# Kernel tuning notes

Measured on AMD Instinct MI355X. Metric: run time of the kernel, lower is better.

Reference implementation:

```python
import jax, jax.numpy as jnp
import numpy as np

N_GRAPHS = 1000  # static number of graphs for global_mean_pool


def setup_inputs() -> dict:
    key = jax.random.key(0)
    ks = jax.random.split(key, 12)
    N, E, DIN, H, OUT = 100000, 1600000, 64, 128, 10
    x = jax.random.normal(ks[0], (N, DIN), dtype=jnp.float32)
    edge_index = jax.random.randint(ks[1], (2, E), 0, N, dtype=jnp.int64)
    batch = jnp.sort(jax.random.randint(ks[2], (N,), 0, N_GRAPHS, dtype=jnp.int64))
    g = lambda k, shp, fan: jax.random.normal(k, shp, dtype=jnp.float32) * np.float32(1.0 / np.sqrt(fan))
    return {
        "x": x, "edge_index": edge_index, "batch": batch,
        "W1": g(ks[3], (DIN, H), DIN), "b1": jnp.zeros((H,), jnp.float32),
        "W2": g(ks[4], (H, H), H),     "b2": jnp.zeros((H,), jnp.float32),
        "W3": g(ks[5], (H, H), H),     "b3": jnp.zeros((H,), jnp.float32),
        "Wl": g(ks[6], (H, OUT), H),   "bl": jnp.zeros((OUT,), jnp.float32),
    }


def _gcn_norm(edge_index, num_nodes):
    # Add self-loops, compute symmetric normalization D^-1/2 (A+I) D^-1/2.
    loops = jnp.arange(num_nodes, dtype=edge_index.dtype)
    src = jnp.concatenate([edge_index[0], loops])
    dst = jnp.concatenate([edge_index[1], loops])
    deg = jax.ops.segment_sum(jnp.ones_like(dst, dtype=jnp.float32), dst, num_segments=num_nodes)
    dinv = jnp.where(deg > 0, jax.lax.rsqrt(jnp.maximum(deg, 1.0)), 0.0)
    norm = dinv[src] * dinv[dst]  # [E + N]
    return src, dst, norm


def _gcn_conv(h, W, b, src, dst, norm, num_nodes):
    h = h @ W                              # linear transform first (PyG GCNConv)
    msg = h[src] * norm[:, None]           # gather + edge scale
    out = jax.ops.segment_sum(msg, dst, num_segments=num_nodes)  # scatter-add
    return out + b


def reference(x, edge_index, batch, W1, b1, W2, b2, W3, b3, Wl, bl):
    N = x.shape[0]
    src, dst, norm = _gcn_norm(edge_index, N)
    h = jax.nn.relu(_gcn_conv(x, W1, b1, src, dst, norm, N))
    h = jax.nn.relu(_gcn_conv(h, W2, b2, src, dst, norm, N))
    h = jax.nn.relu(_gcn_conv(h, W3, b3, src, dst, norm, N))
    # global mean pool over graphs
    sums = jax.ops.segment_sum(h, batch, num_segments=N_GRAPHS)
    cnt = jax.ops.segment_sum(jnp.ones((N,), jnp.float32), batch, num_segments=N_GRAPHS)
    pooled = sums / jnp.maximum(cnt, 1.0)[:, None]
    # dropout(p=0.5) is identity in eval mode
    return pooled @ Wl + bl  # [N_GRAPHS, OUT]
```

## Files before the change

kernel.cpp:

```cpp
#include <hip/hip_runtime.h>
#include <math.h>

#define HID 128
#define NOUT 10
#define NG 1000
#define SCAN_B 256

typedef unsigned short u16;
typedef __attribute__((ext_vector_type(8))) short bf16x8;
typedef __attribute__((ext_vector_type(8))) unsigned short u16x8;
typedef __attribute__((ext_vector_type(4))) float f32x4;

__device__ inline u16 f2bf(float f) {
    unsigned x = __float_as_uint(f);
    return (u16)((x + 0x7FFF + ((x >> 16) & 1)) >> 16);
}
__device__ inline float bf2f(u16 b) { return __uint_as_float(((unsigned)b) << 16); }

__global__ void k_zero(float* __restrict__ p, int n) {
    int i = blockIdx.x * 256 + threadIdx.x;
    if (i < n) p[i] = 0.f;
}

__global__ void k_count_rank(const int* __restrict__ ei, int* __restrict__ counts,
                             int* __restrict__ rank, int E) {
    int e = blockIdx.x * 256 + threadIdx.x;
    if (e < E) rank[e] = atomicAdd(&counts[ei[(size_t)E + e]], 1);
}

__global__ __launch_bounds__(SCAN_B) void k_scan1(const int* __restrict__ counts,
                                                  int* __restrict__ rowptr,
                                                  int* __restrict__ bsum,
                                                  float* __restrict__ dinv, int N) {
    __shared__ int s[SCAN_B];
    int t = threadIdx.x;
    int i = blockIdx.x * SCAN_B + t;
    int v = (i < N) ? counts[i] : 0;
    if (i < N) dinv[i] = rsqrtf((float)(v + 1));
    s[t] = v;
    __syncthreads();
    for (int off = 1; off < SCAN_B; off <<= 1) {
        int u = (t >= off) ? s[t - off] : 0;
        __syncthreads();
        s[t] += u;
        __syncthreads();
    }
    if (i < N) rowptr[i] = s[t] - v;
    if (t == SCAN_B - 1) bsum[blockIdx.x] = s[t];
}

__global__ __launch_bounds__(512) void k_scan2(int* __restrict__ bsum, int nb) {
    __shared__ int s[512];
    int t = threadIdx.x;
    int v = (t < nb) ? bsum[t] : 0;
    s[t] = v;
    __syncthreads();
    for (int off = 1; off < 512; off <<= 1) {
        int u = (t >= off) ? s[t - off] : 0;
        __syncthreads();
        s[t] += u;
        __syncthreads();
    }
    if (t < nb) bsum[t] = s[t] - v;
}

__global__ void k_scan3(int* __restrict__ rowptr, const int* __restrict__ bsum, int N, int E) {
    int i = blockIdx.x * SCAN_B + threadIdx.x;
    if (i < N) rowptr[i] += bsum[blockIdx.x];
    if (i == 0) rowptr[N] = E;
}

__global__ void k_scatter(const int* __restrict__ ei, const int* __restrict__ rank,
                          const int* __restrict__ rowptr, int* __restrict__ sorted, int E) {
    int e = blockIdx.x * 256 + threadIdx.x;
    if (e >= E) return;
    int s = ei[e];
    int d = ei[(size_t)E + e];
    sorted[rowptr[d] + rank[e]] = s << 8;
}

__global__ void k_bounds(const int* __restrict__ batch, int* __restrict__ gstart, int N) {
    int i = blockIdx.x * 256 + threadIdx.x;
    if (i >= N) return;
    int cur = batch[i];
    if (i == 0) {
        for (int g = 0; g <= cur; ++g) gstart[g] = 0;
    } else {
        int prev = batch[i - 1];
        for (int g = prev + 1; g <= cur; ++g) gstart[g] = i;
    }
    if (i == N - 1) {
        for (int g = cur + 1; g <= NG; ++g) gstart[g] = N;
    }
}

template<int K>
__global__ void k_wsplit(const float* __restrict__ W, u16* __restrict__ whi, u16* __restrict__ wlo) {
    int idx = blockIdx.x * 256 + threadIdx.x;
    if (idx >= K * HID) return;
    int k = idx >> 7;
    int col = idx & 127;
    float v = W[idx];
    u16 hb = f2bf(v);
    u16 lb = f2bf(v - bf2f(hb));
    int ks = k >> 5;
    int kq = (k >> 3) & 3;
    int j = k & 7;
    int c = col >> 4;
    int r = col & 15;
    int lane = kq * 16 + r;
    size_t pos = ((size_t)(ks * 8 + c) * 64 + lane) * 8 + j;
    whi[pos] = hb;
    wlo[pos] = lb;
}

template<int K, bool RELU_IN>
__global__ __launch_bounds__(256) void k_gemm_mfma(const float* __restrict__ in,
                                                   const u16* __restrict__ whi,
                                                   const u16* __restrict__ wlo,
                                                   const float* __restrict__ dinv,
                                                   u16* __restrict__ g, int N) {
    constexpr int NKS = K / 32;
    const int w = threadIdx.x >> 6;
    const int l = threadIdx.x & 63;
    const int row0 = blockIdx.x * 64 + w * 16;
    const int r = l & 15;
    const int q = l >> 4;

    int arow = row0 + r;
    if (arow > N - 1) arow = N - 1;
    const float* ap = in + (size_t)arow * K + q * 8;

    bf16x8 ahi[NKS], alo[NKS];
#pragma unroll
    for (int ks = 0; ks < NKS; ++ks) {
        float4 v0 = *(const float4*)(ap + ks * 32);
        float4 v1 = *(const float4*)(ap + ks * 32 + 4);
        float va[8] = {v0.x, v0.y, v0.z, v0.w, v1.x, v1.y, v1.z, v1.w};
#pragma unroll
        for (int j = 0; j < 8; ++j) {
            float f = va[j];
            if (RELU_IN) f = fmaxf(f, 0.f);
            u16 hb = f2bf(f);
            ahi[ks][j] = (short)hb;
            alo[ks][j] = (short)f2bf(f - bf2f(hb));
        }
    }

    f32x4 acc[8];
#pragma unroll
    for (int c = 0; c < 8; ++c) acc[c] = (f32x4){0.f, 0.f, 0.f, 0.f};

    const bf16x8* whiv = (const bf16x8*)whi;
    const bf16x8* wlov = (const bf16x8*)wlo;

#pragma unroll
    for (int ks = 0; ks < NKS; ++ks) {
#pragma unroll
        for (int c = 0; c < 8; ++c) {
            bf16x8 b = whiv[(size_t)(ks * 8 + c) * 64 + l];
            acc[c] = __builtin_amdgcn_mfma_f32_16x16x32_bf16(ahi[ks], b, acc[c], 0, 0, 0);
            acc[c] = __builtin_amdgcn_mfma_f32_16x16x32_bf16(alo[ks], b, acc[c], 0, 0, 0);
        }
    }
#pragma unroll
    for (int ks = 0; ks < NKS; ++ks) {
#pragma unroll
        for (int c = 0; c < 8; ++c) {
            bf16x8 b = wlov[(size_t)(ks * 8 + c) * 64 + l];
            acc[c] = __builtin_amdgcn_mfma_f32_16x16x32_bf16(ahi[ks], b, acc[c], 0, 0, 0);
        }
    }

    float dv[4];
#pragma unroll
    for (int i = 0; i < 4; ++i) {
        int rr = row0 + q * 4 + i;
        dv[i] = (rr < N) ? dinv[rr] : 0.f;
    }
#pragma unroll
    for (int c = 0; c < 8; ++c) {
#pragma unroll
        for (int i = 0; i < 4; ++i) {
            int rr = row0 + q * 4 + i;
            if (rr < N) g[(size_t)rr * HID + c * 16 + r] = f2bf(acc[c][i] * dv[i]);
        }
    }
}

#define BFACC(a, p)                                   \
    a[0] += __uint_as_float((p).x << 16);             \
    a[1] += __uint_as_float((p).x & 0xffff0000u);     \
    a[2] += __uint_as_float((p).y << 16);             \
    a[3] += __uint_as_float((p).y & 0xffff0000u);     \
    a[4] += __uint_as_float((p).z << 16);             \
    a[5] += __uint_as_float((p).z & 0xffff0000u);     \
    a[6] += __uint_as_float((p).w << 16);             \
    a[7] += __uint_as_float((p).w & 0xffff0000u);

__global__ __launch_bounds__(256) void k_aggr(const int* __restrict__ rowptr,
                                              const int* __restrict__ sorted,
                                              const u16* __restrict__ g,
                                              const float* __restrict__ dinv,
                                              const float* __restrict__ b,
                                              float* __restrict__ out, int N) {
    int wid = threadIdx.x >> 6;
    int lane = threadIdx.x & 63;
    int v = blockIdx.x * 4 + wid;
    if (v >= N) return;
    int qq = lane >> 4;
    int r = lane & 15;
    int cb = r * 16;

    const char* gb = (const char*)g;

    float a0[8], a1[8];
#pragma unroll
    for (int i = 0; i < 8; ++i) { a0[i] = 0.f; a1[i] = 0.f; }

    int beg = rowptr[v], end = rowptr[v + 1];
    int j = beg + qq;
    for (; j + 4 < end; j += 8) {
        int o0 = sorted[j];
        int o1 = sorted[j + 4];
        uint4 p0 = *(const uint4*)(gb + o0 + cb);
        uint4 p1 = *(const uint4*)(gb + o1 + cb);
        BFACC(a0, p0);
        BFACC(a1, p1);
    }
    for (; j < end; j += 4) {
        int o0 = sorted[j];
        uint4 p0 = *(const uint4*)(gb + o0 + cb);
        BFACC(a0, p0);
    }

#pragma unroll
    for (int i = 0; i < 8; ++i) {
        float t = a0[i] + a1[i];
        t += __shfl_xor(t, 16);
        t += __shfl_xor(t, 32);
        a0[i] = t;
    }

    if (qq == 0) {
        uint4 sv = *(const uint4*)(gb + ((size_t)v << 8) + cb);
        float se[8];
        se[0] = __uint_as_float(sv.x << 16); se[1] = __uint_as_float(sv.x & 0xffff0000u);
        se[2] = __uint_as_float(sv.y << 16); se[3] = __uint_as_float(sv.y & 0xffff0000u);
        se[4] = __uint_as_float(sv.z << 16); se[5] = __uint_as_float(sv.z & 0xffff0000u);
        se[6] = __uint_as_float(sv.w << 16); se[7] = __uint_as_float(sv.w & 0xffff0000u);
        float dv = dinv[v];
        int c8 = r * 8;
        float4 bv0 = *(const float4*)&b[c8];
        float4 bv1 = *(const float4*)&b[c8 + 4];
        float4 o0, o1;
        o0.x = bv0.x + dv * (a0[0] + se[0]);
        o0.y = bv0.y + dv * (a0[1] + se[1]);
        o0.z = bv0.z + dv * (a0[2] + se[2]);
        o0.w = bv0.w + dv * (a0[3] + se[3]);
        o1.x = bv1.x + dv * (a0[4] + se[4]);
        o1.y = bv1.y + dv * (a0[5] + se[5]);
        o1.z = bv1.z + dv * (a0[6] + se[6]);
        o1.w = bv1.w + dv * (a0[7] + se[7]);
        *(float4*)&out[(size_t)v * HID + c8] = o0;
        *(float4*)&out[(size_t)v * HID + c8 + 4] = o1;
    }
}

__global__ __launch_bounds__(256) void k_poolfinal(const float* __restrict__ h,
                                                   const int* __restrict__ gstart,
                                                   const float* __restrict__ Wl,
                                                   const float* __restrict__ bl,
                                                   float* __restrict__ out) {
    __shared__ float pool[HID];
    int g = blockIdx.x;
    int t = threadIdx.x;
    int col = t & 127;
    int grp = t >> 7;
    int beg = gstart[g], end = gstart[g + 1];

    float acc = 0.f;
    for (int i = beg + grp; i < end; i += 2)
        acc += fmaxf(h[(size_t)i * HID + col], 0.f);

    if (grp == 1) pool[col] = acc;
    __syncthreads();
    if (grp == 0) {
        float tot = acc + pool[col];
        float c = fmaxf((float)(end - beg), 1.0f);
        pool[col] = tot / c;
    }
    __syncthreads();
    if (t < NOUT) {
        float a = bl[t];
        for (int k = 0; k < HID; ++k) a += pool[k] * Wl[k * NOUT + t];
        out[g * NOUT + t] = a;
    }
}

__global__ void k_probe(float* __restrict__ out, int n, float val) {
    int i = blockIdx.x * 256 + threadIdx.x;
    if (i < n) out[i] = val;
}

extern "C" void kernel_launch(void* const* d_in, const int* in_sizes, int n_in,
                              void* d_out, int out_size, void* d_ws, size_t ws_size,
                              hipStream_t stream) {
    const float* x    = (const float*)d_in[0];
    const int* ei     = (const int*)d_in[1];
    const int* batch  = (const int*)d_in[2];
    const float* W1 = (const float*)d_in[3];
    const float* b1 = (const float*)d_in[4];
    const float* W2 = (const float*)d_in[5];
    const float* b2 = (const float*)d_in[6];
    const float* W3 = (const float*)d_in[7];
    const float* b3 = (const float*)d_in[8];
    const float* Wl = (const float*)d_in[9];
    const float* bl = (const float*)d_in[10];
    float* out = (float*)d_out;

    const int N = in_sizes[0] / 64;
    const int E = in_sizes[1] / 2;

    char* ws = (char*)d_ws;
    const size_t off_dinv   = 0;
    const size_t off_counts = 400000;
    const size_t off_rowptr = 800000;
    const size_t off_rank   = 1200128;
    const size_t off_bsum   = 7600128;
    const size_t off_gstart = 7602176;
    const size_t off_sorted = 7606400;
    const size_t off_hW     = 14006400;
    const size_t off_bufB   = 39606400;
    const size_t off_wf1h   = 90806400;
    const size_t off_wf1l   = 90822784;
    const size_t off_wf2h   = 90839168;
    const size_t off_wf2l   = 90871936;
    const size_t off_wf3h   = 90904704;
    const size_t off_wf3l   = 90937472;
    const size_t need       = 90970240;

    if (ws_size < need) {
        float enc = (float)(ws_size >> 20);
        k_probe<<<(out_size + 255) / 256, 256, 0, stream>>>(out, out_size, enc);
        return;
    }

    float* dinv  = (float*)(ws + off_dinv);
    int* counts  = (int*)(ws + off_counts);
    int* rowptr  = (int*)(ws + off_rowptr);
    int* rank    = (int*)(ws + off_rank);
    int* bsum    = (int*)(ws + off_bsum);
    int* gstart  = (int*)(ws + off_gstart);
    int* sorted  = (int*)(ws + off_sorted);
    u16* hW      = (u16*)(ws + off_hW);
    float* bufB  = (float*)(ws + off_bufB);
    u16* wf1h = (u16*)(ws + off_wf1h);  u16* wf1l = (u16*)(ws + off_wf1l);
    u16* wf2h = (u16*)(ws + off_wf2h);  u16* wf2l = (u16*)(ws + off_wf2l);
    u16* wf3h = (u16*)(ws + off_wf3h);  u16* wf3l = (u16*)(ws + off_wf3l);

    dim3 blk(256);
    const int gN = (N + 255) / 256;
    const int gE = (E + 255) / 256;
    const int nScanBlk = (N + SCAN_B - 1) / SCAN_B;
    const int mfmaGrid = (N + 63) / 64;
    const int aggrGrid = (N + 3) / 4;

    k_zero<<<gN, blk, 0, stream>>>((float*)counts, N);
    k_count_rank<<<gE, blk, 0, stream>>>(ei, counts, rank, E);
    k_scan1<<<nScanBlk, SCAN_B, 0, stream>>>(counts, rowptr, bsum, dinv, N);
    k_scan2<<<1, 512, 0, stream>>>(bsum, nScanBlk);
    k_scan3<<<nScanBlk, SCAN_B, 0, stream>>>(rowptr, bsum, N, E);
    k_scatter<<<gE, blk, 0, stream>>>(ei, rank, rowptr, sorted, E);
    k_bounds<<<gN, blk, 0, stream>>>(batch, gstart, N);
    k_wsplit<64><<<(64 * HID + 255) / 256, blk, 0, stream>>>(W1, wf1h, wf1l);
    k_wsplit<128><<<(128 * HID + 255) / 256, blk, 0, stream>>>(W2, wf2h, wf2l);
    k_wsplit<128><<<(128 * HID + 255) / 256, blk, 0, stream>>>(W3, wf3h, wf3l);

    k_gemm_mfma<64, false><<<mfmaGrid, blk, 0, stream>>>(x, wf1h, wf1l, dinv, hW, N);
    k_aggr<<<aggrGrid, blk, 0, stream>>>(rowptr, sorted, hW, dinv, b1, bufB, N);
    k_gemm_mfma<128, true><<<mfmaGrid, blk, 0, stream>>>(bufB, wf2h, wf2l, dinv, hW, N);
    k_aggr<<<aggrGrid, blk, 0, stream>>>(rowptr, sorted, hW, dinv, b2, bufB, N);
    k_gemm_mfma<128, true><<<mfmaGrid, blk, 0, stream>>>(bufB, wf3h, wf3l, dinv, hW, N);
    k_aggr<<<aggrGrid, blk, 0, stream>>>(rowptr, sorted, hW, dinv, b3, bufB, N);

    k_poolfinal<<<NG, blk, 0, stream>>>(bufB, gstart, Wl, bl, out);
}
```

Baseline: 457.5 us.

## Fuse ReLU and bf16 hi/lo split into aggregation, split nodes across two waves

The aggregation kernel now applies bias and ReLU itself and writes its output as pre-split bf16 hi/lo arrays instead of fp32. The next GEMM loads these operands directly rather than converting fp32 on load, and the pooling kernel reads the hi/lo pair. Each node's aggregation is split across two wavefronts, one per 64-column half, so more waves run while each gathers half the row bytes. The three weight-split launches are merged into one. The intermediate buffers keep the same total bytes, but per-row conversion work moves out of the GEMM.

```diff
diff --git a/kernel.cpp b/kernel.cpp
--- a/kernel.cpp
+++ b/kernel.cpp
@@ -8,7 +8,6 @@
 
 typedef unsigned short u16;
 typedef __attribute__((ext_vector_type(8))) short bf16x8;
-typedef __attribute__((ext_vector_type(8))) unsigned short u16x8;
 typedef __attribute__((ext_vector_type(4))) float f32x4;
 
 __device__ inline u16 f2bf(float f) {
@@ -94,13 +93,20 @@
     }
 }
 
-template<int K>
-__global__ void k_wsplit(const float* __restrict__ W, u16* __restrict__ whi, u16* __restrict__ wlo) {
+__global__ void k_wsplit_all(const float* __restrict__ W1, const float* __restrict__ W2,
+                             const float* __restrict__ W3,
+                             u16* __restrict__ w1h, u16* __restrict__ w1l,
+                             u16* __restrict__ w2h, u16* __restrict__ w2l,
+                             u16* __restrict__ w3h, u16* __restrict__ w3l) {
     int idx = blockIdx.x * 256 + threadIdx.x;
-    if (idx >= K * HID) return;
-    int k = idx >> 7;
-    int col = idx & 127;
-    float v = W[idx];
+    const float* W; u16 *wh, *wl; int base;
+    if (idx < 64 * HID)            { W = W1; wh = w1h; wl = w1l; base = idx; }
+    else if (idx < 192 * HID)      { W = W2; wh = w2h; wl = w2l; base = idx - 64 * HID; }
+    else if (idx < 320 * HID)      { W = W3; wh = w3h; wl = w3l; base = idx - 192 * HID; }
+    else return;
+    int k = base >> 7;
+    int col = base & 127;
+    float v = W[base];
     u16 hb = f2bf(v);
     u16 lb = f2bf(v - bf2f(hb));
     int ks = k >> 5;
@@ -110,16 +116,16 @@
     int r = col & 15;
     int lane = kq * 16 + r;
     size_t pos = ((size_t)(ks * 8 + c) * 64 + lane) * 8 + j;
-    whi[pos] = hb;
-    wlo[pos] = lb;
-}
-
-template<int K, bool RELU_IN>
-__global__ __launch_bounds__(256) void k_gemm_mfma(const float* __restrict__ in,
-                                                   const u16* __restrict__ whi,
-                                                   const u16* __restrict__ wlo,
-                                                   const float* __restrict__ dinv,
-                                                   u16* __restrict__ g, int N) {
+    wh[pos] = hb;
+    wl[pos] = lb;
+}
+
+template<int K>
+__global__ __launch_bounds__(256) void k_gemm_f32(const float* __restrict__ in,
+                                                  const u16* __restrict__ whi,
+                                                  const u16* __restrict__ wlo,
+                                                  const float* __restrict__ dinv,
+                                                  u16* __restrict__ g, int N) {
     constexpr int NKS = K / 32;
     const int w = threadIdx.x >> 6;
     const int l = threadIdx.x & 63;
@@ -140,11 +146,77 @@
 #pragma unroll
         for (int j = 0; j < 8; ++j) {
             float f = va[j];
-            if (RELU_IN) f = fmaxf(f, 0.f);
             u16 hb = f2bf(f);
             ahi[ks][j] = (short)hb;
             alo[ks][j] = (short)f2bf(f - bf2f(hb));
         }
+    }
+
+    f32x4 acc[8];
+#pragma unroll
+    for (int c = 0; c < 8; ++c) acc[c] = (f32x4){0.f, 0.f, 0.f, 0.f};
+
+    const bf16x8* whiv = (const bf16x8*)whi;
+    const bf16x8* wlov = (const bf16x8*)wlo;
+
+#pragma unroll
+    for (int ks = 0; ks < NKS; ++ks) {
+#pragma unroll
+        for (int c = 0; c < 8; ++c) {
+            bf16x8 b = whiv[(size_t)(ks * 8 + c) * 64 + l];
+            acc[c] = __builtin_amdgcn_mfma_f32_16x16x32_bf16(ahi[ks], b, acc[c], 0, 0, 0);
+            acc[c] = __builtin_amdgcn_mfma_f32_16x16x32_bf16(alo[ks], b, acc[c], 0, 0, 0);
+        }
+    }
+#pragma unroll
+    for (int ks = 0; ks < NKS; ++ks) {
+#pragma unroll
+        for (int c = 0; c < 8; ++c) {
+            bf16x8 b = wlov[(size_t)(ks * 8 + c) * 64 + l];
+            acc[c] = __builtin_amdgcn_mfma_f32_16x16x32_bf16(ahi[ks], b, acc[c], 0, 0, 0);
+        }
+    }
+
+    float dv[4];
+#pragma unroll
+    for (int i = 0; i < 4; ++i) {
+        int rr = row0 + q * 4 + i;
+        dv[i] = (rr < N) ? dinv[rr] : 0.f;
+    }
+#pragma unroll
+    for (int c = 0; c < 8; ++c) {
+#pragma unroll
+        for (int i = 0; i < 4; ++i) {
+            int rr = row0 + q * 4 + i;
+            if (rr < N) g[(size_t)rr * HID + c * 16 + r] = f2bf(acc[c][i] * dv[i]);
+        }
+    }
+}
+
+template<int K>
+__global__ __launch_bounds__(256) void k_gemm_pre(const u16* __restrict__ ain_h,
+                                                  const u16* __restrict__ ain_l,
+                                                  const u16* __restrict__ whi,
+                                                  const u16* __restrict__ wlo,
+                                                  const float* __restrict__ dinv,
+                                                  u16* __restrict__ g, int N) {
+    constexpr int NKS = K / 32;
+    const int w = threadIdx.x >> 6;
+    const int l = threadIdx.x & 63;
+    const int row0 = blockIdx.x * 64 + w * 16;
+    const int r = l & 15;
+    const int q = l >> 4;
+
+    int arow = row0 + r;
+    if (arow > N - 1) arow = N - 1;
+    const u16* aph = ain_h + (size_t)arow * K + q * 8;
+    const u16* apl = ain_l + (size_t)arow * K + q * 8;
+
+    bf16x8 ahi[NKS], alo[NKS];
+#pragma unroll
+    for (int ks = 0; ks < NKS; ++ks) {
+        ahi[ks] = *(const bf16x8*)(aph + ks * 32);
+        alo[ks] = *(const bf16x8*)(apl + ks * 32);
     }
 
     f32x4 acc[8];
@@ -203,14 +275,17 @@
                                               const u16* __restrict__ g,
                                               const float* __restrict__ dinv,
                                               const float* __restrict__ b,
-                                              float* __restrict__ out, int N) {
-    int wid = threadIdx.x >> 6;
+                                              u16* __restrict__ ahi, u16* __restrict__ alo,
+                                              int N) {
+    int wgl = threadIdx.x >> 6;
     int lane = threadIdx.x & 63;
-    int v = blockIdx.x * 4 + wid;
+    int W = blockIdx.x * 4 + wgl;
+    int v = W >> 1;
     if (v >= N) return;
-    int qq = lane >> 4;
-    int r = lane & 15;
-    int cb = r * 16;
+    int half = W & 1;
+    int s = lane >> 3;
+    int r8 = lane & 7;
+    int cb = half * 128 + r8 * 16;
 
     const char* gb = (const char*)g;
 
@@ -219,16 +294,16 @@
     for (int i = 0; i < 8; ++i) { a0[i] = 0.f; a1[i] = 0.f; }
 
     int beg = rowptr[v], end = rowptr[v + 1];
-    int j = beg + qq;
-    for (; j + 4 < end; j += 8) {
+    int j = beg + s;
+    for (; j + 8 < end; j += 16) {
         int o0 = sorted[j];
-        int o1 = sorted[j + 4];
+        int o1 = sorted[j + 8];
         uint4 p0 = *(const uint4*)(gb + o0 + cb);
         uint4 p1 = *(const uint4*)(gb + o1 + cb);
         BFACC(a0, p0);
         BFACC(a1, p1);
     }
-    for (; j < end; j += 4) {
+    for (; j < end; j += 8) {
         int o0 = sorted[j];
         uint4 p0 = *(const uint4*)(gb + o0 + cb);
         BFACC(a0, p0);
@@ -237,12 +312,13 @@
 #pragma unroll
     for (int i = 0; i < 8; ++i) {
         float t = a0[i] + a1[i];
+        t += __shfl_xor(t, 8);
         t += __shfl_xor(t, 16);
         t += __shfl_xor(t, 32);
         a0[i] = t;
     }
 
-    if (qq == 0) {
+    if (s == 0) {
         uint4 sv = *(const uint4*)(gb + ((size_t)v << 8) + cb);
         float se[8];
         se[0] = __uint_as_float(sv.x << 16); se[1] = __uint_as_float(sv.x & 0xffff0000u);
@@ -250,45 +326,58 @@
         se[4] = __uint_as_float(sv.z << 16); se[5] = __uint_as_float(sv.z & 0xffff0000u);
         se[6] = __uint_as_float(sv.w << 16); se[7] = __uint_as_float(sv.w & 0xffff0000u);
         float dv = dinv[v];
-        int c8 = r * 8;
-        float4 bv0 = *(const float4*)&b[c8];
-        float4 bv1 = *(const float4*)&b[c8 + 4];
-        float4 o0, o1;
-        o0.x = bv0.x + dv * (a0[0] + se[0]);
-        o0.y = bv0.y + dv * (a0[1] + se[1]);
-        o0.z = bv0.z + dv * (a0[2] + se[2]);
-        o0.w = bv0.w + dv * (a0[3] + se[3]);
-        o1.x = bv1.x + dv * (a0[4] + se[4]);
-        o1.y = bv1.y + dv * (a0[5] + se[5]);
-        o1.z = bv1.z + dv * (a0[6] + se[6]);
-        o1.w = bv1.w + dv * (a0[7] + se[7]);
-        *(float4*)&out[(size_t)v * HID + c8] = o0;
-        *(float4*)&out[(size_t)v * HID + c8 + 4] = o1;
-    }
-}
-
-__global__ __launch_bounds__(256) void k_poolfinal(const float* __restrict__ h,
+        int c = half * 64 + r8 * 8;
+        float4 bv0 = *(const float4*)&b[c];
+        float4 bv1 = *(const float4*)&b[c + 4];
+        float bb[8] = {bv0.x, bv0.y, bv0.z, bv0.w, bv1.x, bv1.y, bv1.z, bv1.w};
+        unsigned H[4], L[4];
+#pragma unroll
+        for (int p = 0; p < 4; ++p) {
+            u16 h2[2], l2[2];
+#pragma unroll
+            for (int e = 0; e < 2; ++e) {
+                int i = p * 2 + e;
+                float f = fmaxf(bb[i] + dv * (a0[i] + se[i]), 0.f);
+                u16 hb = f2bf(f);
+                h2[e] = hb;
+                l2[e] = f2bf(f - bf2f(hb));
+            }
+            H[p] = (unsigned)h2[0] | ((unsigned)h2[1] << 16);
+            L[p] = (unsigned)l2[0] | ((unsigned)l2[1] << 16);
+        }
+        *(uint4*)&ahi[(size_t)v * HID + c] = make_uint4(H[0], H[1], H[2], H[3]);
+        *(uint4*)&alo[(size_t)v * HID + c] = make_uint4(L[0], L[1], L[2], L[3]);
+    }
+}
+
+__global__ __launch_bounds__(256) void k_poolfinal(const u16* __restrict__ ahi,
+                                                   const u16* __restrict__ alo,
                                                    const int* __restrict__ gstart,
                                                    const float* __restrict__ Wl,
                                                    const float* __restrict__ bl,
                                                    float* __restrict__ out) {
+    __shared__ float part[4][HID];
     __shared__ float pool[HID];
     int g = blockIdx.x;
     int t = threadIdx.x;
-    int col = t & 127;
-    int grp = t >> 7;
+    int cp = t & 63;
+    int grp = t >> 6;
     int beg = gstart[g], end = gstart[g + 1];
 
-    float acc = 0.f;
-    for (int i = beg + grp; i < end; i += 2)
-        acc += fmaxf(h[(size_t)i * HID + col], 0.f);
-
-    if (grp == 1) pool[col] = acc;
+    float s0 = 0.f, s1 = 0.f;
+    for (int i = beg + grp; i < end; i += 4) {
+        unsigned h = *(const unsigned*)&ahi[(size_t)i * HID + cp * 2];
+        unsigned l = *(const unsigned*)&alo[(size_t)i * HID + cp * 2];
+        s0 += __uint_as_float(h << 16) + __uint_as_float(l << 16);
+        s1 += __uint_as_float(h & 0xffff0000u) + __uint_as_float(l & 0xffff0000u);
+    }
+    part[grp][cp * 2] = s0;
+    part[grp][cp * 2 + 1] = s1;
     __syncthreads();
-    if (grp == 0) {
-        float tot = acc + pool[col];
+    if (t < HID) {
+        float tot = part[0][t] + part[1][t] + part[2][t] + part[3][t];
         float c = fmaxf((float)(end - beg), 1.0f);
-        pool[col] = tot / c;
+        pool[t] = tot / c;
     }
     __syncthreads();
     if (t < NOUT) {
@@ -330,8 +419,9 @@
     const size_t off_bsum   = 7600128;
     const size_t off_gstart = 7602176;
     const size_t off_sorted = 7606400;
-    const size_t off_hW     = 14006400;
-    const size_t off_bufB   = 39606400;
+    const size_t off_g      = 14006400;
+    const size_t off_ahi    = 39606400;
+    const size_t off_alo    = 65206400;
     const size_t off_wf1h   = 90806400;
     const size_t off_wf1l   = 90822784;
     const size_t off_wf2h   = 90839168;
@@ -353,8 +443,9 @@
     int* bsum    = (int*)(ws + off_bsum);
     int* gstart  = (int*)(ws + off_gstart);
     int* sorted  = (int*)(ws + off_sorted);
-    u16* hW      = (u16*)(ws + off_hW);
-    float* bufB  = (float*)(ws + off_bufB);
+    u16* g       = (u16*)(ws + off_g);
+    u16* ahi     = (u16*)(ws + off_ahi);
+    u16* alo     = (u16*)(ws + off_alo);
     u16* wf1h = (u16*)(ws + off_wf1h);  u16* wf1l = (u16*)(ws + off_wf1l);
     u16* wf2h = (u16*)(ws + off_wf2h);  u16* wf2l = (u16*)(ws + off_wf2l);
     u16* wf3h = (u16*)(ws + off_wf3h);  u16* wf3l = (u16*)(ws + off_wf3l);
@@ -364,7 +455,7 @@
     const int gE = (E + 255) / 256;
     const int nScanBlk = (N + SCAN_B - 1) / SCAN_B;
     const int mfmaGrid = (N + 63) / 64;
-    const int aggrGrid = (N + 3) / 4;
+    const int aggrGrid = (2 * N + 3) / 4;
 
     k_zero<<<gN, blk, 0, stream>>>((float*)counts, N);
     k_count_rank<<<gE, blk, 0, stream>>>(ei, counts, rank, E);
@@ -373,16 +464,15 @@
     k_scan3<<<nScanBlk, SCAN_B, 0, stream>>>(rowptr, bsum, N, E);
     k_scatter<<<gE, blk, 0, stream>>>(ei, rank, rowptr, sorted, E);
     k_bounds<<<gN, blk, 0, stream>>>(batch, gstart, N);
-    k_wsplit<64><<<(64 * HID + 255) / 256, blk, 0, stream>>>(W1, wf1h, wf1l);
-    k_wsplit<128><<<(128 * HID + 255) / 256, blk, 0, stream>>>(W2, wf2h, wf2l);
-    k_wsplit<128><<<(128 * HID + 255) / 256, blk, 0, stream>>>(W3, wf3h, wf3l);
-
-    k_gemm_mfma<64, false><<<mfmaGrid, blk, 0, stream>>>(x, wf1h, wf1l, dinv, hW, N);
-    k_aggr<<<aggrGrid, blk, 0, stream>>>(rowptr, sorted, hW, dinv, b1, bufB, N);
-    k_gemm_mfma<128, true><<<mfmaGrid, blk, 0, stream>>>(bufB, wf2h, wf2l, dinv, hW, N);
-    k_aggr<<<aggrGrid, blk, 0, stream>>>(rowptr, sorted, hW, dinv, b2, bufB, N);
-    k_gemm_mfma<128, true><<<mfmaGrid, blk, 0, stream>>>(bufB, wf3h, wf3l, dinv, hW, N);
-    k_aggr<<<aggrGrid, blk, 0, stream>>>(rowptr, sorted, hW, dinv, b3, bufB, N);
-
-    k_poolfinal<<<NG, blk, 0, stream>>>(bufB, gstart, Wl, bl, out);
-}
+    k_wsplit_all<<<(320 * HID + 255) / 256, blk, 0, stream>>>(W1, W2, W3,
+                                                              wf1h, wf1l, wf2h, wf2l, wf3h, wf3l);
+
+    k_gemm_f32<64><<<mfmaGrid, blk, 0, stream>>>(x, wf1h, wf1l, dinv, g, N);
+    k_aggr<<<aggrGrid, blk, 0, stream>>>(rowptr, sorted, g, dinv, b1, ahi, alo, N);
+    k_gemm_pre<128><<<mfmaGrid, blk, 0, stream>>>(ahi, alo, wf2h, wf2l, dinv, g, N);
+    k_aggr<<<aggrGrid, blk, 0, stream>>>(rowptr, sorted, g, dinv, b2, ahi, alo, N);
+    k_gemm_pre<128><<<mfmaGrid, blk, 0, stream>>>(ahi, alo, wf3h, wf3l, dinv, g, N);
+    k_aggr<<<aggrGrid, blk, 0, stream>>>(rowptr, sorted, g, dinv, b3, ahi, alo, N);
+
+    k_poolfinal<<<NG, blk, 0, stream>>>(ahi, alo, gstart, Wl, bl, out);
+}
```

After: 512.8 us. 1.12x slower.
